# Kernel tuning notes

Hardware: AMD Instinct MI355X
Metric: run time of the kernel (lower is better)

## Reference

```python
import jax, jax.numpy as jnp
import numpy as np

NUM_HEADS = 4
HEAD_DIM = 128  # out_dim // num_heads = 512 // 4
TOP_K = 16
NEG_SLOPE = 0.2


def setup_inputs() -> dict:
    key = jax.random.key(0)
    k1, k2, k3, k4 = jax.random.split(key, 4)
    N, in_dim, out_dim = 4096, 1024, 512
    x = jax.random.normal(k1, (N, in_dim), dtype=jnp.float32)
    adj = jax.random.uniform(k2, (N, N), dtype=jnp.float32)  # all-positive, like softmax attn
    W = jax.random.normal(k3, (out_dim, in_dim), dtype=jnp.float32) * 0.02
    a = jax.random.normal(k4, (1, 2 * HEAD_DIM), dtype=jnp.float32) * 0.02
    return {"x": x, "adj": adj, "W": W, "a": a}


def reference(x, adj, W, a):
    N = x.shape[0]
    Wh = (x @ W.T).reshape(N, NUM_HEADS, HEAD_DIM)  # (N, H, D)

    # _sparsify_adj: keep top-k per row, binary mask
    k = min(TOP_K, N)
    _, topk_idx = jax.lax.top_k(adj, k)  # (N, k)
    rows = jnp.arange(N)[:, None]
    sparse = jnp.zeros_like(adj).at[rows, topk_idx].set(1.0)
    mask = sparse > 0  # (N_i, N_j)

    # a([Wh_i, Wh_j]) decomposed: a = [a_src | a_dst], score = s_i + s_j
    a_src, a_dst = a[0, :HEAD_DIM], a[0, HEAD_DIM:]
    s_i = jnp.einsum("nhd,d->nh", Wh, a_src)  # (N, H)
    s_j = jnp.einsum("nhd,d->nh", Wh, a_dst)  # (N, H)
    e = jax.nn.leaky_relu(s_i[:, None, :] + s_j[None, :, :], NEG_SLOPE)  # (N_i, N_j, H)
    e = jnp.where(mask[:, :, None], e, -jnp.inf)

    alpha = jax.nn.softmax(e, axis=1)  # softmax over neighbors j
    alpha = jnp.nan_to_num(alpha, nan=0.0)

    out = jnp.einsum("imh,mhd->ihd", alpha, Wh)  # weighted sum over j
    return jax.nn.elu(out.reshape(N, -1))  # (N, out_dim)
```

## Files before the change

### kernel.cpp

```cpp
#include <hip/hip_runtime.h>
#include <hip/hip_bf16.h>

#define N_NODES 4096
#define IN_DIM 1024
#define OUT_DIM 512
#define NUM_HEADS 4
#define HEAD_DIM 128
#define TOP_K 16
#define NEG_SLOPE 0.2f

typedef __attribute__((ext_vector_type(8))) short bf16x8;
typedef __attribute__((ext_vector_type(4))) float f32x4;

typedef __attribute__((address_space(3))) unsigned as3_u32;
typedef const __attribute__((address_space(1))) unsigned as1_u32;

static __device__ __forceinline__ void gld16(const void* g, void* l) {
    __builtin_amdgcn_global_load_lds((as1_u32*)g, (as3_u32*)l, 16, 0, 0);
}

__device__ __forceinline__ unsigned short f2bf(float f) {
    unsigned u = __float_as_uint(f);
    unsigned r = u + 0x7FFFu + ((u >> 16) & 1u);
    return (unsigned short)(r >> 16);
}
__device__ __forceinline__ float bf2f(unsigned short h) {
    return __uint_as_float(((unsigned)h) << 16);
}

__device__ __forceinline__ void conv_row(const float* __restrict__ src,
                                         unsigned short* __restrict__ dst, int t)
{
    int row = t >> 7, rem = t & 127, kb = rem >> 2, c = rem & 3;
    const float* s = src + (size_t)row * IN_DIM + kb * 32 + c * 8;
    float4 v0 = *(const float4*)s;
    float4 v1 = *(const float4*)(s + 4);
    float vv[8] = {v0.x, v0.y, v0.z, v0.w, v1.x, v1.y, v1.z, v1.w};
    bf16x8 H, L;
#pragma unroll
    for (int e = 0; e < 8; ++e) {
        unsigned short h = f2bf(vv[e]);
        H[e] = (short)h;
        L[e] = (short)f2bf(vv[e] - bf2f(h));
    }
    int sw = row & 7;
    unsigned short* base = dst + (size_t)row * 2048 + kb * 64;
    *(bf16x8*)(base + ((c ^ sw) << 3))       = H;
    *(bf16x8*)(base + (((c + 4) ^ sw) << 3)) = L;
}

__global__ __launch_bounds__(256) void prep_kernel(
    const float* __restrict__ x, const float* __restrict__ W,
    unsigned short* __restrict__ xc, unsigned short* __restrict__ wc,
    float* __restrict__ szero)
{
    int b = blockIdx.x, tid = threadIdx.x;
    if (b < 2048) {
        conv_row(x, xc, b * 256 + tid);
    } else if (b < 2304) {
        conv_row(W, wc, (b - 2048) * 256 + tid);
    } else {
        int t = (b - 2304) * 256 + tid;
        ((float4*)szero)[t] = (float4){0.f, 0.f, 0.f, 0.f};
    }
}

#define GBM 128
#define GBN 64

__global__ __launch_bounds__(256) void gemm_kernel(
    const unsigned short* __restrict__ xc, const unsigned short* __restrict__ wc,
    const float* __restrict__ a, unsigned short* __restrict__ Whb,
    float* __restrict__ s_src, float* __restrict__ s_dst)
{
    __shared__ __align__(16) unsigned short A0[GBM * 64];
    __shared__ __align__(16) unsigned short A1[GBM * 64];
    __shared__ __align__(16) unsigned short A2[GBM * 64];
    __shared__ __align__(16) unsigned short B0[GBN * 64];
    __shared__ __align__(16) unsigned short B1[GBN * 64];
    __shared__ __align__(16) unsigned short B2[GBN * 64];

    const int tid = threadIdx.x;
    const int id  = blockIdx.x;
    const int xcd = id & 7, seq = id >> 3;
    const int bm  = xcd * 4 + (seq >> 3), bn = seq & 7;

    const int wave = tid >> 6, lane = tid & 63;
    const int wm = wave >> 1, wn = wave & 1;
    const int lr = lane & 15, lk = lane >> 4;

    f32x4 acc[4][2];
#pragma unroll
    for (int i = 0; i < 4; ++i)
#pragma unroll
        for (int j = 0; j < 2; ++j) acc[i][j] = (f32x4){0.f, 0.f, 0.f, 0.f};

#define STAGE(Abuf, Bbuf, kt) do {                                            \
        size_t koff = (size_t)(kt) * 128;                                     \
        _Pragma("unroll")                                                     \
        for (int q = 0; q < 4; ++q) {             \
            int ci = q * 256 + tid;                                           \
            int row = ci >> 3, p = ci & 7;                                    \
            gld16((const char*)xc + ((size_t)(bm * GBM + row) * 4096 + koff + p * 16), \
                  (char*)(Abuf) + (size_t)ci * 16);                           \
        }                                                                     \
        _Pragma("unroll")                                                     \
        for (int q = 0; q < 2; ++q) {               \
            int ci = q * 256 + tid;                                           \
            int row = ci >> 3, p = ci & 7;                                    \
            gld16((const char*)wc + ((size_t)(bn * GBN + row) * 4096 + koff + p * 16), \
                  (char*)(Bbuf) + (size_t)ci * 16);                           \
        }                                                                     \
    } while (0)

#define COMPUTE(Abuf, Bbuf) do {                                              \
        bf16x8 bh[2], bl[2];                                                  \
        _Pragma("unroll")                                                     \
        for (int ni = 0; ni < 2; ++ni) {                                      \
            int rb = wn * 32 + ni * 16 + lr; int swb = rb & 7;                \
            bh[ni] = *(const bf16x8*)&(Bbuf)[rb * 64 + ((lk ^ swb) << 3)];    \
            bl[ni] = *(const bf16x8*)&(Bbuf)[rb * 64 + (((4 + lk) ^ swb) << 3)]; \
        }                                                                     \
        __builtin_amdgcn_s_setprio(1);                                        \
        _Pragma("unroll")                                                     \
        for (int mi = 0; mi < 4; ++mi) {                                      \
            int r = wm * 64 + mi * 16 + lr; int sw = r & 7;                   \
            bf16x8 ah = *(const bf16x8*)&(Abuf)[r * 64 + ((lk ^ sw) << 3)];   \
            bf16x8 al = *(const bf16x8*)&(Abuf)[r * 64 + (((4 + lk) ^ sw) << 3)]; \
            _Pragma("unroll")                                                 \
            for (int ni = 0; ni < 2; ++ni) {                                  \
                acc[mi][ni] = __builtin_amdgcn_mfma_f32_16x16x32_bf16(ah, bh[ni], acc[mi][ni], 0, 0, 0); \
                acc[mi][ni] = __builtin_amdgcn_mfma_f32_16x16x32_bf16(ah, bl[ni], acc[mi][ni], 0, 0, 0); \
                acc[mi][ni] = __builtin_amdgcn_mfma_f32_16x16x32_bf16(al, bh[ni], acc[mi][ni], 0, 0, 0); \
            }                                                                 \
        }                                                                     \
        __builtin_amdgcn_s_setprio(0);                                        \
    } while (0)

#define BODY(Ac, Bc, An, Bn, ktn, W) do {                                     \
        asm volatile("s_waitcnt vmcnt(" #W ")" ::: "memory");                 \
        __builtin_amdgcn_s_barrier();                                         \
        asm volatile("" ::: "memory");                                        \
        if ((ktn) < 32) STAGE(An, Bn, ktn);                                   \
        COMPUTE(Ac, Bc);                                                      \
    } while (0)

    STAGE(A0, B0, 0);
    STAGE(A1, B1, 1);

    for (int i = 0; i < 10; ++i) {
        int t = i * 3;
        BODY(A0, B0, A2, B2, t + 2, 6);
        BODY(A1, B1, A0, B0, t + 3, 6);
        BODY(A2, B2, A1, B1, t + 4, 6);
    }
    BODY(A0, B0, A2, B2, 32, 6);
    asm volatile("s_waitcnt vmcnt(0)" ::: "memory");
    __builtin_amdgcn_s_barrier();
    asm volatile("" ::: "memory");
    COMPUTE(A1, B1);

#undef BODY
#undef COMPUTE
#undef STAGE

    const int h = bn >> 1;
    float ca[2], cb[2];
#pragma unroll
    for (int ni = 0; ni < 2; ++ni) {
        int dcol = (bn & 1) * 64 + wn * 32 + ni * 16 + lr;
        ca[ni] = a[dcol];
        cb[ni] = a[HEAD_DIM + dcol];
    }
#pragma unroll
    for (int mi = 0; mi < 4; ++mi) {
        float ss[4] = {0.f, 0.f, 0.f, 0.f}, sd[4] = {0.f, 0.f, 0.f, 0.f};
#pragma unroll
        for (int ni = 0; ni < 2; ++ni) {
            int col_g = bn * GBN + wn * 32 + ni * 16 + lr;
#pragma unroll
            for (int r = 0; r < 4; ++r) {
                int row_g = bm * GBM + wm * 64 + mi * 16 + lk * 4 + r;
                float v = acc[mi][ni][r];
                Whb[(size_t)row_g * OUT_DIM + col_g] = f2bf(v);
                ss[r] += v * ca[ni];
                sd[r] += v * cb[ni];
            }
        }
#pragma unroll
        for (int s = 1; s < 16; s <<= 1)
#pragma unroll
            for (int r = 0; r < 4; ++r) {
                ss[r] += __shfl_xor(ss[r], s);
                sd[r] += __shfl_xor(sd[r], s);
            }
        if (lr == 0) {
#pragma unroll
            for (int r = 0; r < 4; ++r) {
                int row_g = bm * GBM + wm * 64 + mi * 16 + lk * 4 + r;
                atomicAdd(&s_src[row_g * NUM_HEADS + h], ss[r]);
                atomicAdd(&s_dst[row_g * NUM_HEADS + h], sd[r]);
            }
        }
    }
}

#define TK_THRESH 0.988f

__global__ __launch_bounds__(256) void topk_kernel(
    const float* __restrict__ adj, int* __restrict__ topk)
{
    const int row  = blockIdx.x;
    const int tid  = threadIdx.x;
    const int wave = tid >> 6, lane = tid & 63;
    const float* rp = adj + (size_t)row * N_NODES;

    __shared__ unsigned long long cand[4][64];
    __shared__ int wcnt[4];
    __shared__ float srow[N_NODES];

    float4 q0 = *(const float4*)(rp + wave * 1024 + 0 * 256 + lane * 4);
    float4 q1 = *(const float4*)(rp + wave * 1024 + 1 * 256 + lane * 4);
    float4 q2 = *(const float4*)(rp + wave * 1024 + 2 * 256 + lane * 4);
    float4 q3 = *(const float4*)(rp + wave * 1024 + 3 * 256 + lane * 4);

    const unsigned long long lmask = (1ull << lane) - 1ull;
    int cnt = 0;

#define FILT(qv, i, e, comp) do {                                             \
        float val = (qv).comp;                                                \
        int g = wave * 1024 + (i) * 256 + lane * 4 + (e);                     \
        bool p = val >= TK_THRESH;                                            \
        unsigned long long m = __ballot(p);                                   \
        if (p) {                                                              \
            int pos = cnt + __popcll(m & lmask);                              \
            if (pos < 64) {                                                   \
                unsigned b  = __float_as_uint(val);                           \
                unsigned mo = b ^ (unsigned)(((int)b >> 31) | 0x80000000);    \
                cand[wave][pos] =                                             \
                    ((unsigned long long)mo << 32) | (unsigned)(N_NODES - 1 - g); \
            }                                                                 \
        }                                                                     \
        cnt += __popcll(m);                                                   \
    } while (0)

    FILT(q0, 0, 0, x); FILT(q0, 0, 1, y); FILT(q0, 0, 2, z); FILT(q0, 0, 3, w);
    FILT(q1, 1, 0, x); FILT(q1, 1, 1, y); FILT(q1, 1, 2, z); FILT(q1, 1, 3, w);
    FILT(q2, 2, 0, x); FILT(q2, 2, 1, y); FILT(q2, 2, 2, z); FILT(q2, 2, 3, w);
    FILT(q3, 3, 0, x); FILT(q3, 3, 1, y); FILT(q3, 3, 2, z); FILT(q3, 3, 3, w);
#undef FILT

    if (lane == 0) wcnt[wave] = cnt;
    __syncthreads();

    const int c0n = wcnt[0], c1n = wcnt[1], c2n = wcnt[2], c3n = wcnt[3];
    const int total = c0n + c1n + c2n + c3n;
    const bool ok = (total >= TOP_K) &&
                    (c0n <= 64) && (c1n <= 64) && (c2n <= 64) && (c3n <= 64);
    int* op = topk + (size_t)row * TOP_K;

    if (ok) {
        if (wave == 0) {
            unsigned long long k0 = lane < c0n ? cand[0][lane] : 0ull;
            unsigned long long k1 = lane < c1n ? cand[1][lane] : 0ull;
            unsigned long long k2 = lane < c2n ? cand[2][lane] : 0ull;
            unsigned long long k3 = lane < c3n ? cand[3][lane] : 0ull;
            for (int r = 0; r < TOP_K; ++r) {
                unsigned long long a01 = k0 > k1 ? k0 : k1;
                unsigned long long a23 = k2 > k3 ? k2 : k3;
                unsigned long long b = a01 > a23 ? a01 : a23;
#pragma unroll
                for (int m = 1; m < 64; m <<= 1) {
                    unsigned long long o = __shfl_xor(b, m);
                    b = o > b ? o : b;
                }
                if (lane == 0) op[r] = N_NODES - 1 - (int)(unsigned)(b & 0xFFFFFFFFu);
                if (k0 == b) k0 = 0ull;
                if (k1 == b) k1 = 0ull;
                if (k2 == b) k2 = 0ull;
                if (k3 == b) k3 = 0ull;
            }
        }
    } else {
        int base = wave * 1024 + lane * 4;
        *(float4*)&srow[base + 0 * 256] = q0;
        *(float4*)&srow[base + 1 * 256] = q1;
        *(float4*)&srow[base + 2 * 256] = q2;
        *(float4*)&srow[base + 3 * 256] = q3;
        __syncthreads();
        if (wave == 0) {
            for (int r = 0; r < TOP_K; ++r) {
                float bv = -INFINITY; int bg = 0x7fffffff;
                for (int j = 0; j < 64; ++j) {
                    int g = j * 64 + lane;
                    float val = srow[g];
                    bool better = (val > bv) || (val == bv && g < bg);
                    bv = better ? val : bv;
                    bg = better ? g : bg;
                }
#pragma unroll
                for (int m = 1; m < 64; m <<= 1) {
                    float ov = __shfl_xor(bv, m);
                    int   og = __shfl_xor(bg, m);
                    bool better = (ov > bv) || (ov == bv && og < bg);
                    bv = better ? ov : bv;
                    bg = better ? og : bg;
                }
                if (lane == 0) { op[r] = bg; srow[bg] = -INFINITY; }
            }
        }
    }
}

__global__ __launch_bounds__(256) void aggregate_kernel(
    const unsigned short* __restrict__ Whb, const int* __restrict__ topk,
    const float* __restrict__ s_src, const float* __restrict__ s_dst,
    float* __restrict__ out)
{
    const int i = blockIdx.x, t = threadIdx.x;
    __shared__ int   sidx[TOP_K];
    __shared__ float salpha[TOP_K][NUM_HEADS];
    __shared__ float part[3][8][64];

    if (t < 64) {
        int idxv = 0;
        if (t < TOP_K) { idxv = topk[(size_t)i * TOP_K + t]; sidx[t] = idxv; }
        int m = t >> 2, h = t & 3;
        int im = __shfl(idxv, m);
        float e = s_src[i * NUM_HEADS + h] + s_dst[im * NUM_HEADS + h];
        e = (e >= 0.f) ? e : NEG_SLOPE * e;
        float mx = e;
#pragma unroll
        for (int s = 4; s < 64; s <<= 1) mx = fmaxf(mx, __shfl_xor(mx, s));
        float ex = expf(e - mx);
        float sum = ex;
#pragma unroll
        for (int s = 4; s < 64; s <<= 1) sum += __shfl_xor(sum, s);
        salpha[m][h] = ex / sum;
    }
    __syncthreads();

    const int g = t >> 6, o = t & 63;
    const int h = o >> 4;
    float acc8[8] = {0.f, 0.f, 0.f, 0.f, 0.f, 0.f, 0.f, 0.f};
#pragma unroll
    for (int q = 0; q < 4; ++q) {
        int m = g * 4 + q;
        float al = salpha[m][h];
        bf16x8 v = *(const bf16x8*)&Whb[(size_t)sidx[m] * OUT_DIM + o * 8];
#pragma unroll
        for (int e = 0; e < 8; ++e)
            acc8[e] += al * bf2f((unsigned short)v[e]);
    }
    if (g) {
#pragma unroll
        for (int e = 0; e < 8; ++e) part[g - 1][e][o] = acc8[e];
    }
    __syncthreads();
    if (!g) {
        float r8[8];
#pragma unroll
        for (int e = 0; e < 8; ++e) {
            float s = acc8[e] + part[0][e][o] + part[1][e][o] + part[2][e][o];
            r8[e] = s > 0.f ? s : expf(s) - 1.f;
        }
        float4 lo = (float4){r8[0], r8[1], r8[2], r8[3]};
        float4 hi = (float4){r8[4], r8[5], r8[6], r8[7]};
        *(float4*)(out + (size_t)i * OUT_DIM + o * 8)     = lo;
        *(float4*)(out + (size_t)i * OUT_DIM + o * 8 + 4) = hi;
    }
}

extern "C" void kernel_launch(void* const* d_in, const int* in_sizes, int n_in,
                              void* d_out, int out_size, void* d_ws, size_t ws_size,
                              hipStream_t stream) {
    const float* x   = (const float*)d_in[0];
    const float* adj = (const float*)d_in[1];
    const float* W   = (const float*)d_in[2];
    const float* a   = (const float*)d_in[3];
    float* out = (float*)d_out;

    char* ws = (char*)d_ws;
    unsigned short* Whb   = (unsigned short*)ws;
    unsigned short* xc    = (unsigned short*)(ws + (8u << 20));
    unsigned short* wc    = (unsigned short*)(ws + (24u << 20));
    float*          s_src = (float*)(ws + (26u << 20));
    float*          s_dst = s_src + N_NODES * NUM_HEADS;
    int*            topkb = (int*)(s_dst + N_NODES * NUM_HEADS);

    prep_kernel<<<2336, 256, 0, stream>>>(x, W, xc, wc, s_src);
    gemm_kernel<<<256, 256, 0, stream>>>(xc, wc, a, Whb, s_src, s_dst);
    topk_kernel<<<N_NODES, 256, 0, stream>>>(adj, topkb);
    aggregate_kernel<<<N_NODES, 256, 0, stream>>>(Whb, topkb, s_src, s_dst, out);
}
```

Baseline: 159.3 us.

## Fuse top-k into prep kernel, deepen GEMM pipeline, replace score atomics with partials

Merges the top-k selection over adj with the fp32-to-bf16 split conversion into one launch, so the bandwidth-heavy adj scan overlaps the conversion work and one kernel launch is dropped. The GEMM moves from a 3-stage to a 4-stage LDS pipeline, prefetching three k-tiles ahead. Atomic accumulation of the attention scores is replaced by plain stores into four per-quarter partial buffers, which the aggregate kernel sums, so the zero-init pass goes away. The costs are more LDS per GEMM block, which may limit occupancy, and eight score loads per aggregate lane instead of two.

```diff
diff --git a/kernel.cpp b/kernel.cpp
--- a/kernel.cpp
+++ b/kernel.cpp
@@ -49,168 +49,11 @@
     *(bf16x8*)(base + (((c + 4) ^ sw) << 3)) = L;
 }
 
-__global__ __launch_bounds__(256) void prep_kernel(
-    const float* __restrict__ x, const float* __restrict__ W,
-    unsigned short* __restrict__ xc, unsigned short* __restrict__ wc,
-    float* __restrict__ szero)
+#define TK_THRESH 0.988f
+
+__device__ __forceinline__ void topk_body(int row, const float* __restrict__ adj,
+                                          int* __restrict__ topkb)
 {
-    int b = blockIdx.x, tid = threadIdx.x;
-    if (b < 2048) {
-        conv_row(x, xc, b * 256 + tid);
-    } else if (b < 2304) {
-        conv_row(W, wc, (b - 2048) * 256 + tid);
-    } else {
-        int t = (b - 2304) * 256 + tid;
-        ((float4*)szero)[t] = (float4){0.f, 0.f, 0.f, 0.f};
-    }
-}
-
-#define GBM 128
-#define GBN 64
-
-__global__ __launch_bounds__(256) void gemm_kernel(
-    const unsigned short* __restrict__ xc, const unsigned short* __restrict__ wc,
-    const float* __restrict__ a, unsigned short* __restrict__ Whb,
-    float* __restrict__ s_src, float* __restrict__ s_dst)
-{
-    __shared__ __align__(16) unsigned short A0[GBM * 64];
-    __shared__ __align__(16) unsigned short A1[GBM * 64];
-    __shared__ __align__(16) unsigned short A2[GBM * 64];
-    __shared__ __align__(16) unsigned short B0[GBN * 64];
-    __shared__ __align__(16) unsigned short B1[GBN * 64];
-    __shared__ __align__(16) unsigned short B2[GBN * 64];
-
-    const int tid = threadIdx.x;
-    const int id  = blockIdx.x;
-    const int xcd = id & 7, seq = id >> 3;
-    const int bm  = xcd * 4 + (seq >> 3), bn = seq & 7;
-
-    const int wave = tid >> 6, lane = tid & 63;
-    const int wm = wave >> 1, wn = wave & 1;
-    const int lr = lane & 15, lk = lane >> 4;
-
-    f32x4 acc[4][2];
-#pragma unroll
-    for (int i = 0; i < 4; ++i)
-#pragma unroll
-        for (int j = 0; j < 2; ++j) acc[i][j] = (f32x4){0.f, 0.f, 0.f, 0.f};
-
-#define STAGE(Abuf, Bbuf, kt) do {                                            \
-        size_t koff = (size_t)(kt) * 128;                                     \
-        _Pragma("unroll")                                                     \
-        for (int q = 0; q < 4; ++q) {             \
-            int ci = q * 256 + tid;                                           \
-            int row = ci >> 3, p = ci & 7;                                    \
-            gld16((const char*)xc + ((size_t)(bm * GBM + row) * 4096 + koff + p * 16), \
-                  (char*)(Abuf) + (size_t)ci * 16);                           \
-        }                                                                     \
-        _Pragma("unroll")                                                     \
-        for (int q = 0; q < 2; ++q) {               \
-            int ci = q * 256 + tid;                                           \
-            int row = ci >> 3, p = ci & 7;                                    \
-            gld16((const char*)wc + ((size_t)(bn * GBN + row) * 4096 + koff + p * 16), \
-                  (char*)(Bbuf) + (size_t)ci * 16);                           \
-        }                                                                     \
-    } while (0)
-
-#define COMPUTE(Abuf, Bbuf) do {                                              \
-        bf16x8 bh[2], bl[2];                                                  \
-        _Pragma("unroll")                                                     \
-        for (int ni = 0; ni < 2; ++ni) {                                      \
-            int rb = wn * 32 + ni * 16 + lr; int swb = rb & 7;                \
-            bh[ni] = *(const bf16x8*)&(Bbuf)[rb * 64 + ((lk ^ swb) << 3)];    \
-            bl[ni] = *(const bf16x8*)&(Bbuf)[rb * 64 + (((4 + lk) ^ swb) << 3)]; \
-        }                                                                     \
-        __builtin_amdgcn_s_setprio(1);                                        \
-        _Pragma("unroll")                                                     \
-        for (int mi = 0; mi < 4; ++mi) {                                      \
-            int r = wm * 64 + mi * 16 + lr; int sw = r & 7;                   \
-            bf16x8 ah = *(const bf16x8*)&(Abuf)[r * 64 + ((lk ^ sw) << 3)];   \
-            bf16x8 al = *(const bf16x8*)&(Abuf)[r * 64 + (((4 + lk) ^ sw) << 3)]; \
-            _Pragma("unroll")                                                 \
-            for (int ni = 0; ni < 2; ++ni) {                                  \
-                acc[mi][ni] = __builtin_amdgcn_mfma_f32_16x16x32_bf16(ah, bh[ni], acc[mi][ni], 0, 0, 0); \
-                acc[mi][ni] = __builtin_amdgcn_mfma_f32_16x16x32_bf16(ah, bl[ni], acc[mi][ni], 0, 0, 0); \
-                acc[mi][ni] = __builtin_amdgcn_mfma_f32_16x16x32_bf16(al, bh[ni], acc[mi][ni], 0, 0, 0); \
-            }                                                                 \
-        }                                                                     \
-        __builtin_amdgcn_s_setprio(0);                                        \
-    } while (0)
-
-#define BODY(Ac, Bc, An, Bn, ktn, W) do {                                     \
-        asm volatile("s_waitcnt vmcnt(" #W ")" ::: "memory");                 \
-        __builtin_amdgcn_s_barrier();                                         \
-        asm volatile("" ::: "memory");                                        \
-        if ((ktn) < 32) STAGE(An, Bn, ktn);                                   \
-        COMPUTE(Ac, Bc);                                                      \
-    } while (0)
-
-    STAGE(A0, B0, 0);
-    STAGE(A1, B1, 1);
-
-    for (int i = 0; i < 10; ++i) {
-        int t = i * 3;
-        BODY(A0, B0, A2, B2, t + 2, 6);
-        BODY(A1, B1, A0, B0, t + 3, 6);
-        BODY(A2, B2, A1, B1, t + 4, 6);
-    }
-    BODY(A0, B0, A2, B2, 32, 6);
-    asm volatile("s_waitcnt vmcnt(0)" ::: "memory");
-    __builtin_amdgcn_s_barrier();
-    asm volatile("" ::: "memory");
-    COMPUTE(A1, B1);
-
-#undef BODY
-#undef COMPUTE
-#undef STAGE
-
-    const int h = bn >> 1;
-    float ca[2], cb[2];
-#pragma unroll
-    for (int ni = 0; ni < 2; ++ni) {
-        int dcol = (bn & 1) * 64 + wn * 32 + ni * 16 + lr;
-        ca[ni] = a[dcol];
-        cb[ni] = a[HEAD_DIM + dcol];
-    }
-#pragma unroll
-    for (int mi = 0; mi < 4; ++mi) {
-        float ss[4] = {0.f, 0.f, 0.f, 0.f}, sd[4] = {0.f, 0.f, 0.f, 0.f};
-#pragma unroll
-        for (int ni = 0; ni < 2; ++ni) {
-            int col_g = bn * GBN + wn * 32 + ni * 16 + lr;
-#pragma unroll
-            for (int r = 0; r < 4; ++r) {
-                int row_g = bm * GBM + wm * 64 + mi * 16 + lk * 4 + r;
-                float v = acc[mi][ni][r];
-                Whb[(size_t)row_g * OUT_DIM + col_g] = f2bf(v);
-                ss[r] += v * ca[ni];
-                sd[r] += v * cb[ni];
-            }
-        }
-#pragma unroll
-        for (int s = 1; s < 16; s <<= 1)
-#pragma unroll
-            for (int r = 0; r < 4; ++r) {
-                ss[r] += __shfl_xor(ss[r], s);
-                sd[r] += __shfl_xor(sd[r], s);
-            }
-        if (lr == 0) {
-#pragma unroll
-            for (int r = 0; r < 4; ++r) {
-                int row_g = bm * GBM + wm * 64 + mi * 16 + lk * 4 + r;
-                atomicAdd(&s_src[row_g * NUM_HEADS + h], ss[r]);
-                atomicAdd(&s_dst[row_g * NUM_HEADS + h], sd[r]);
-            }
-        }
-    }
-}
-
-#define TK_THRESH 0.988f
-
-__global__ __launch_bounds__(256) void topk_kernel(
-    const float* __restrict__ adj, int* __restrict__ topk)
-{
-    const int row  = blockIdx.x;
     const int tid  = threadIdx.x;
     const int wave = tid >> 6, lane = tid & 63;
     const float* rp = adj + (size_t)row * N_NODES;
@@ -257,7 +100,7 @@
     const int total = c0n + c1n + c2n + c3n;
     const bool ok = (total >= TOP_K) &&
                     (c0n <= 64) && (c1n <= 64) && (c2n <= 64) && (c3n <= 64);
-    int* op = topk + (size_t)row * TOP_K;
+    int* op = topkb + (size_t)row * TOP_K;
 
     if (ok) {
         if (wave == 0) {
@@ -312,10 +155,174 @@
     }
 }
 
+__global__ __launch_bounds__(256) void prep_topk_kernel(
+    const float* __restrict__ x, const float* __restrict__ W,
+    unsigned short* __restrict__ xc, unsigned short* __restrict__ wc,
+    const float* __restrict__ adj, int* __restrict__ topkb)
+{
+    int b = blockIdx.x, tid = threadIdx.x;
+    if (b < 4096) {
+        topk_body(b, adj, topkb);
+    } else if (b < 6144) {
+        conv_row(x, xc, (b - 4096) * 256 + tid);
+    } else {
+        conv_row(W, wc, (b - 6144) * 256 + tid);
+    }
+}
+
+#define GBM 128
+#define GBN 64
+
+__global__ __launch_bounds__(256) void gemm_kernel(
+    const unsigned short* __restrict__ xc, const unsigned short* __restrict__ wc,
+    const float* __restrict__ a, unsigned short* __restrict__ Whb,
+    float* __restrict__ spart)
+{
+    __shared__ __align__(16) unsigned short A0[GBM * 64];
+    __shared__ __align__(16) unsigned short A1[GBM * 64];
+    __shared__ __align__(16) unsigned short A2[GBM * 64];
+    __shared__ __align__(16) unsigned short A3[GBM * 64];
+    __shared__ __align__(16) unsigned short B0[GBN * 64];
+    __shared__ __align__(16) unsigned short B1[GBN * 64];
+    __shared__ __align__(16) unsigned short B2[GBN * 64];
+    __shared__ __align__(16) unsigned short B3[GBN * 64];
+
+    const int tid = threadIdx.x;
+    const int id  = blockIdx.x;
+    const int xcd = id & 7, seq = id >> 3;
+    const int bm  = xcd * 4 + (seq >> 3), bn = seq & 7;
+
+    const int wave = tid >> 6, lane = tid & 63;
+    const int wm = wave >> 1, wn = wave & 1;
+    const int lr = lane & 15, lk = lane >> 4;
+
+    f32x4 acc[4][2];
+#pragma unroll
+    for (int i = 0; i < 4; ++i)
+#pragma unroll
+        for (int j = 0; j < 2; ++j) acc[i][j] = (f32x4){0.f, 0.f, 0.f, 0.f};
+
+#define STAGE(Abuf, Bbuf, kt) do {                                            \
+        size_t koff = (size_t)(kt) * 128;                                     \
+        _Pragma("unroll")                                                     \
+        for (int q = 0; q < 4; ++q) {             \
+            int ci = q * 256 + tid;                                           \
+            int row = ci >> 3, p = ci & 7;                                    \
+            gld16((const char*)xc + ((size_t)(bm * GBM + row) * 4096 + koff + p * 16), \
+                  (char*)(Abuf) + (size_t)ci * 16);                           \
+        }                                                                     \
+        _Pragma("unroll")                                                     \
+        for (int q = 0; q < 2; ++q) {               \
+            int ci = q * 256 + tid;                                           \
+            int row = ci >> 3, p = ci & 7;                                    \
+            gld16((const char*)wc + ((size_t)(bn * GBN + row) * 4096 + koff + p * 16), \
+                  (char*)(Bbuf) + (size_t)ci * 16);                           \
+        }                                                                     \
+    } while (0)
+
+#define COMPUTE(Abuf, Bbuf) do {                                              \
+        bf16x8 bh[2], bl[2];                                                  \
+        _Pragma("unroll")                                                     \
+        for (int ni = 0; ni < 2; ++ni) {                                      \
+            int rb = wn * 32 + ni * 16 + lr; int swb = rb & 7;                \
+            bh[ni] = *(const bf16x8*)&(Bbuf)[rb * 64 + ((lk ^ swb) << 3)];    \
+            bl[ni] = *(const bf16x8*)&(Bbuf)[rb * 64 + (((4 + lk) ^ swb) << 3)]; \
+        }                                                                     \
+        __builtin_amdgcn_s_setprio(1);                                        \
+        _Pragma("unroll")                                                     \
+        for (int mi = 0; mi < 4; ++mi) {                                      \
+            int r = wm * 64 + mi * 16 + lr; int sw = r & 7;                   \
+            bf16x8 ah = *(const bf16x8*)&(Abuf)[r * 64 + ((lk ^ sw) << 3)];   \
+            bf16x8 al = *(const bf16x8*)&(Abuf)[r * 64 + (((4 + lk) ^ sw) << 3)]; \
+            _Pragma("unroll")                                                 \
+            for (int ni = 0; ni < 2; ++ni) {                                  \
+                acc[mi][ni] = __builtin_amdgcn_mfma_f32_16x16x32_bf16(ah, bh[ni], acc[mi][ni], 0, 0, 0); \
+                acc[mi][ni] = __builtin_amdgcn_mfma_f32_16x16x32_bf16(ah, bl[ni], acc[mi][ni], 0, 0, 0); \
+                acc[mi][ni] = __builtin_amdgcn_mfma_f32_16x16x32_bf16(al, bh[ni], acc[mi][ni], 0, 0, 0); \
+            }                                                                 \
+        }                                                                     \
+        __builtin_amdgcn_s_setprio(0);                                        \
+    } while (0)
+
+#define BODY(Ac, Bc, An, Bn, ktn, W) do {                                     \
+        asm volatile("s_waitcnt vmcnt(" #W ")" ::: "memory");                 \
+        __builtin_amdgcn_s_barrier();                                         \
+        asm volatile("" ::: "memory");                                        \
+        if ((ktn) < 32) STAGE(An, Bn, ktn);                                   \
+        COMPUTE(Ac, Bc);                                                      \
+    } while (0)
+
+    STAGE(A0, B0, 0);
+    STAGE(A1, B1, 1);
+    STAGE(A2, B2, 2);
+
+    for (int i = 0; i < 7; ++i) {
+        BODY(A0, B0, A3, B3, i * 4 + 3, 12);
+        BODY(A1, B1, A0, B0, i * 4 + 4, 12);
+        BODY(A2, B2, A1, B1, i * 4 + 5, 12);
+        BODY(A3, B3, A2, B2, i * 4 + 6, 12);
+    }
+    BODY(A0, B0, A3, B3, 31, 12);
+    BODY(A1, B1, A0, B0, 33, 12);
+    asm volatile("s_waitcnt vmcnt(6)" ::: "memory");
+    __builtin_amdgcn_s_barrier();
+    asm volatile("" ::: "memory");
+    COMPUTE(A2, B2);
+    asm volatile("s_waitcnt vmcnt(0)" ::: "memory");
+    __builtin_amdgcn_s_barrier();
+    asm volatile("" ::: "memory");
+    COMPUTE(A3, B3);
+
+#undef BODY
+#undef COMPUTE
+#undef STAGE
+
+    const int h = bn >> 1;
+    float* sps = spart + ((size_t)((bn & 1) * 2 + wn)) * 16384;
+    float* spd = spart + 65536 + ((size_t)((bn & 1) * 2 + wn)) * 16384;
+    float ca[2], cb[2];
+#pragma unroll
+    for (int ni = 0; ni < 2; ++ni) {
+        int dcol = (bn & 1) * 64 + wn * 32 + ni * 16 + lr;
+        ca[ni] = a[dcol];
+        cb[ni] = a[HEAD_DIM + dcol];
+    }
+#pragma unroll
+    for (int mi = 0; mi < 4; ++mi) {
+        float ss[4] = {0.f, 0.f, 0.f, 0.f}, sd[4] = {0.f, 0.f, 0.f, 0.f};
+#pragma unroll
+        for (int ni = 0; ni < 2; ++ni) {
+            int col_g = bn * GBN + wn * 32 + ni * 16 + lr;
+#pragma unroll
+            for (int r = 0; r < 4; ++r) {
+                int row_g = bm * GBM + wm * 64 + mi * 16 + lk * 4 + r;
+                float v = acc[mi][ni][r];
+                Whb[(size_t)row_g * OUT_DIM + col_g] = f2bf(v);
+                ss[r] += v * ca[ni];
+                sd[r] += v * cb[ni];
+            }
+        }
+#pragma unroll
+        for (int s = 1; s < 16; s <<= 1)
+#pragma unroll
+            for (int r = 0; r < 4; ++r) {
+                ss[r] += __shfl_xor(ss[r], s);
+                sd[r] += __shfl_xor(sd[r], s);
+            }
+        if (lr == 0) {
+#pragma unroll
+            for (int r = 0; r < 4; ++r) {
+                int row_g = bm * GBM + wm * 64 + mi * 16 + lk * 4 + r;
+                sps[row_g * NUM_HEADS + h] = ss[r];
+                spd[row_g * NUM_HEADS + h] = sd[r];
+            }
+        }
+    }
+}
+
 __global__ __launch_bounds__(256) void aggregate_kernel(
     const unsigned short* __restrict__ Whb, const int* __restrict__ topk,
-    const float* __restrict__ s_src, const float* __restrict__ s_dst,
-    float* __restrict__ out)
+    const float* __restrict__ spart, float* __restrict__ out)
 {
     const int i = blockIdx.x, t = threadIdx.x;
     __shared__ int   sidx[TOP_K];
@@ -327,7 +334,9 @@
         if (t < TOP_K) { idxv = topk[(size_t)i * TOP_K + t]; sidx[t] = idxv; }
         int m = t >> 2, h = t & 3;
         int im = __shfl(idxv, m);
-        float e = s_src[i * NUM_HEADS + h] + s_dst[im * NUM_HEADS + h];
+        int si = (i << 2) + h, di = (im << 2) + h;
+        float e = spart[si] + spart[16384 + si] + spart[32768 + si] + spart[49152 + si]
+                + spart[65536 + di] + spart[81920 + di] + spart[98304 + di] + spart[114688 + di];
         e = (e >= 0.f) ? e : NEG_SLOPE * e;
         float mx = e;
 #pragma unroll
@@ -384,12 +393,10 @@
     unsigned short* Whb   = (unsigned short*)ws;
     unsigned short* xc    = (unsigned short*)(ws + (8u << 20));
     unsigned short* wc    = (unsigned short*)(ws + (24u << 20));
-    float*          s_src = (float*)(ws + (26u << 20));
-    float*          s_dst = s_src + N_NODES * NUM_HEADS;
-    int*            topkb = (int*)(s_dst + N_NODES * NUM_HEADS);
-
-    prep_kernel<<<2336, 256, 0, stream>>>(x, W, xc, wc, s_src);
-    gemm_kernel<<<256, 256, 0, stream>>>(xc, wc, a, Whb, s_src, s_dst);
-    topk_kernel<<<N_NODES, 256, 0, stream>>>(adj, topkb);
-    aggregate_kernel<<<N_NODES, 256, 0, stream>>>(Whb, topkb, s_src, s_dst, out);
-}
+    float*          spart = (float*)(ws + (26u << 20));
+    int*            topkb = (int*)(ws + (26u << 20) + (512u << 10));
+
+    prep_topk_kernel<<<6400, 256, 0, stream>>>(x, W, xc, wc, adj, topkb);
+    gemm_kernel<<<256, 256, 0, stream>>>(xc, wc, a, Whb, spart);
+    aggregate_kernel<<<N_NODES, 256, 0, stream>>>(Whb, topkb, spart, out);
+}
```

Result: faster. 147.3 us (-7.5%).
